# Kernel optimization log

Measured on AMD Instinct MI355X. Metric: run time of the kernel, lower is better.

## Reference

```python
import jax, jax.numpy as jnp
import numpy as np

C = 512
K = 3
DIL1 = 1  # dilation[0]
EPS = 1e-9


def _get_padding(kernel_size, dilation=1):
    return (kernel_size * dilation - dilation) // 2


def _upsample2_linear(x):
    # F.interpolate(x, scale_factor=2, mode='linear', align_corners=False)
    # x: [B, C, T] -> [B, C, 2T]
    T = x.shape[-1]
    coord = (jnp.arange(2 * T, dtype=x.dtype) + 0.5) * 0.5 - 0.5
    coord = jnp.maximum(coord, 0.0)  # PyTorch clamps source coord at 0
    i0 = jnp.floor(coord).astype(jnp.int32)
    i1 = jnp.minimum(i0 + 1, T - 1)
    w1 = coord - i0.astype(x.dtype)
    w0 = 1.0 - w1
    return x[..., i0] * w0 + x[..., i1] * w1


def _downsample2_avg(x):
    # AvgPool1d(kernel_size=2, stride=2)
    B, Ch, T = x.shape
    return x.reshape(B, Ch, T // 2, 2).mean(axis=-1)


def _snakebeta_act1d(x, alpha, beta):
    a = jnp.exp(alpha)[None, :, None]
    b = jnp.exp(beta)[None, :, None]
    up = _upsample2_linear(x)
    y = up + (1.0 - jnp.cos(2.0 * a * up)) / (2.0 * b + EPS)
    return _downsample2_avg(y)


def _wn_weight(v, g):
    # weight_norm: w = g * v / ||v||, norm over (in, k) dims per out channel
    norm = jnp.sqrt(jnp.sum(v * v, axis=(1, 2), keepdims=True))
    return g[:, None, None] * v / norm


def _conv1d(x, w, bias, dilation, pad):
    y = jax.lax.conv_general_dilated(
        x, w, window_strides=(1,), padding=[(pad, pad)],
        rhs_dilation=(dilation,), dimension_numbers=('NCH', 'OIH', 'NCH'))
    return y + bias[None, :, None]


def setup_inputs() -> dict:
    key = jax.random.key(0)
    ks = jax.random.split(key, 11)
    B, T = 8, 8192
    x = jax.random.normal(ks[0], (B, C, T), dtype=jnp.float32)
    v1 = jax.random.normal(ks[1], (C, C, K), dtype=jnp.float32) * 0.05
    g1 = jnp.ones((C,), dtype=jnp.float32)
    bias1 = jax.random.normal(ks[2], (C,), dtype=jnp.float32) * 0.01
    v2 = jax.random.normal(ks[3], (C, C, K), dtype=jnp.float32) * 0.05
    g2 = jnp.ones((C,), dtype=jnp.float32)
    bias2 = jax.random.normal(ks[4], (C,), dtype=jnp.float32) * 0.01
    # SnakeBeta logscale params (init 0 in torch; small random for testing)
    alpha1 = jax.random.normal(ks[5], (C,), dtype=jnp.float32) * 0.1
    beta1 = jax.random.normal(ks[6], (C,), dtype=jnp.float32) * 0.1
    alpha2 = jax.random.normal(ks[7], (C,), dtype=jnp.float32) * 0.1
    beta2 = jax.random.normal(ks[8], (C,), dtype=jnp.float32) * 0.1
    return {"x": x, "v1": v1, "g1": g1, "bias1": bias1,
            "v2": v2, "g2": g2, "bias2": bias2,
            "alpha1": alpha1, "beta1": beta1, "alpha2": alpha2, "beta2": beta2}


def reference(x, v1, g1, bias1, v2, g2, bias2, alpha1, beta1, alpha2, beta2):
    pad1 = _get_padding(K, DIL1)
    pad2 = _get_padding(K, 1)
    xt = _snakebeta_act1d(x, alpha1, beta1)
    xt = _conv1d(xt, _wn_weight(v1, g1), bias1, DIL1, pad1)
    xt = _snakebeta_act1d(xt, alpha2, beta2)
    xt = _conv1d(xt, _wn_weight(v2, g2), bias2, 1, pad2)
    return xt + x[:, :, :xt.shape[2]]
```

## Files before the change

### kernel.cpp

```cpp
#include <hip/hip_runtime.h>

typedef unsigned short ushort_t;
typedef __bf16 bf16x8 __attribute__((ext_vector_type(8)));
typedef float f32x4 __attribute__((ext_vector_type(4)));

#define B_  8
#define C_  512
#define T_  8192
#define TP_ 8194

static __device__ __forceinline__ float bf2f(ushort_t u) {
    return __uint_as_float(((unsigned)u) << 16);
}
static __device__ __forceinline__ ushort_t f2bf(float f) {
    unsigned u = __float_as_uint(f);
    unsigned r = (u + 0x7FFFu + ((u >> 16) & 1u)) >> 16;
    return (ushort_t)r;
}

static __device__ __forceinline__ void gl_lds16(const void* g, void* l) {
    __builtin_amdgcn_global_load_lds(
        (const __attribute__((address_space(1))) void*)g,
        (__attribute__((address_space(3))) void*)l, 16, 0, 0);
}

template <int BF> struct In;
template <> struct In<0> {
    static __device__ __forceinline__ float ld(const void* p, size_t i) {
        return ((const float*)p)[i];
    }
};
template <> struct In<1> {
    static __device__ __forceinline__ float ld(const void* p, size_t i) {
        return bf2f(((const ushort_t*)p)[i]);
    }
};

#define P_G1 0
#define P_B1 512
#define P_G2 1024
#define P_B2 1536
#define P_A1 2048
#define P_I1 2560
#define P_A2 3072
#define P_I2 3584

__global__ void param_kernel(const void* g1, const void* bias1, const void* g2, const void* bias2,
                             const void* alpha1, const void* beta1, const void* alpha2, const void* beta2,
                             float* __restrict__ pr, int* __restrict__ flag) {
    int i = threadIdx.x;
    unsigned guard = ((const unsigned*)g1)[0];
    int bf = (guard == 0x3F803F80u) ? 1 : 0;
    if (i == 0) *flag = bf;
    float g1v, b1v, g2v, b2v, a1v, be1v, a2v, be2v;
    if (bf) {
        g1v = In<1>::ld(g1, i);  b1v = In<1>::ld(bias1, i);
        g2v = In<1>::ld(g2, i);  b2v = In<1>::ld(bias2, i);
        a1v = In<1>::ld(alpha1, i); be1v = In<1>::ld(beta1, i);
        a2v = In<1>::ld(alpha2, i); be2v = In<1>::ld(beta2, i);
    } else {
        g1v = In<0>::ld(g1, i);  b1v = In<0>::ld(bias1, i);
        g2v = In<0>::ld(g2, i);  b2v = In<0>::ld(bias2, i);
        a1v = In<0>::ld(alpha1, i); be1v = In<0>::ld(beta1, i);
        a2v = In<0>::ld(alpha2, i); be2v = In<0>::ld(beta2, i);
    }
    pr[P_G1 + i] = g1v;
    pr[P_B1 + i] = b1v;
    pr[P_G2 + i] = g2v;
    pr[P_B2 + i] = b2v;
    pr[P_A1 + i] = __expf(a1v);
    pr[P_I1 + i] = 1.0f / (2.0f * __expf(be1v) + 1e-9f);
    pr[P_A2 + i] = __expf(a2v);
    pr[P_I2 + i] = 1.0f / (2.0f * __expf(be2v) + 1e-9f);
}

__global__ void wn_kernel(const void* __restrict__ v1, const void* __restrict__ v2,
                          const float* __restrict__ pr, const int* __restrict__ flag,
                          ushort_t* __restrict__ W1, ushort_t* __restrict__ W2) {
    int bf = *flag;
    const void* v = blockIdx.y ? v2 : v1;
    float g = pr[(blockIdx.y ? P_G2 : P_G1) + blockIdx.x];
    ushort_t* W = blockIdx.y ? W2 : W1;
    int co = blockIdx.x;
    int tid = threadIdx.x;
    size_t base = (size_t)co * 1536;
    float vals[6];
    float sum = 0.f;
    if (bf) {
        #pragma unroll
        for (int i = 0; i < 6; ++i) {
            float f = In<1>::ld(v, base + tid + i * 256);
            vals[i] = f;
            sum += f * f;
        }
    } else {
        #pragma unroll
        for (int i = 0; i < 6; ++i) {
            float f = In<0>::ld(v, base + tid + i * 256);
            vals[i] = f;
            sum += f * f;
        }
    }
    #pragma unroll
    for (int o = 32; o > 0; o >>= 1) sum += __shfl_down(sum, o, 64);
    __shared__ float red[4];
    if ((tid & 63) == 0) red[tid >> 6] = sum;
    __syncthreads();
    float tot = red[0] + red[1] + red[2] + red[3];
    float scale = g / sqrtf(tot);
    #pragma unroll
    for (int i = 0; i < 6; ++i) {
        int j = tid + i * 256;
        int cin = j / 3, k = j - cin * 3;
        W[(k * C_ + co) * C_ + cin] = f2bf(vals[i] * scale);
    }
}

__global__ void zero_pad_kernel(ushort_t* __restrict__ h) {
    int i = blockIdx.x * 256 + threadIdx.x;
    int b = i >> 10;
    int r = (i >> 9) & 1;
    int c = i & 511;
    h[((size_t)b * TP_ + (r ? (TP_ - 1) : 0)) * C_ + c] = 0;
}

__global__ void act1_kernel(const void* __restrict__ x,
                            const float* __restrict__ pr, const int* __restrict__ flag,
                            ushort_t* __restrict__ h) {
    __shared__ float s[64][65];
    int bf = *flag;
    int c0 = blockIdx.x * 64, t0 = blockIdx.y * 64, b = blockIdx.z;
    int tid = threadIdx.x;
    int cl = tid >> 2, seg = tid & 3;
    int c = c0 + cl;
    float a = pr[P_A1 + c];
    float inv2b = pr[P_I1 + c];
    size_t xbase = ((size_t)b * C_ + c) << 13;
    int tbase = t0 + seg * 16;
    float xv[18];
    if (bf) {
        const ushort_t* xp = (const ushort_t*)x + xbase;
        #pragma unroll
        for (int q = 0; q < 2; ++q) {
            uint4 v = *(const uint4*)(xp + tbase + q * 8);
            const ushort_t* pv = (const ushort_t*)&v;
            #pragma unroll
            for (int j = 0; j < 8; ++j) xv[1 + q * 8 + j] = bf2f(pv[j]);
        }
        xv[0]  = bf2f(xp[max(tbase - 1, 0)]);
        xv[17] = bf2f(xp[min(tbase + 16, T_ - 1)]);
    } else {
        const float* xp = (const float*)x + xbase;
        #pragma unroll
        for (int q = 0; q < 4; ++q) {
            float4 v = *(const float4*)(xp + tbase + q * 4);
            xv[1 + q * 4 + 0] = v.x;
            xv[1 + q * 4 + 1] = v.y;
            xv[1 + q * 4 + 2] = v.z;
            xv[1 + q * 4 + 3] = v.w;
        }
        xv[0]  = xp[max(tbase - 1, 0)];
        xv[17] = xp[min(tbase + 16, T_ - 1)];
    }
    #pragma unroll
    for (int j = 0; j < 16; ++j) {
        float xm = xv[j], xc = xv[j + 1], xp2 = xv[j + 2];
        float u0 = 0.25f * xm + 0.75f * xc;
        float u1 = 0.75f * xc + 0.25f * xp2;
        float s0 = u0 + (1.0f - __cosf(2.0f * a * u0)) * inv2b;
        float s1 = u1 + (1.0f - __cosf(2.0f * a * u1)) * inv2b;
        s[cl][seg * 16 + j] = 0.5f * (s0 + s1);
    }
    __syncthreads();
    int tl = tid >> 2;
    int t = t0 + tl;
    ushort_t* hrow = h + ((size_t)b * TP_ + (t + 1)) * C_ + c0 + seg * 16;
    #pragma unroll
    for (int q = 0; q < 4; ++q) {
        int cb = seg * 16 + q * 4;
        ushort4 w;
        w.x = f2bf(s[cb + 0][tl]);
        w.y = f2bf(s[cb + 1][tl]);
        w.z = f2bf(s[cb + 2][tl]);
        w.w = f2bf(s[cb + 3][tl]);
        *(ushort4*)(hrow + q * 4) = w;
    }
}

__global__ void act2_kernel(const ushort_t* __restrict__ z,
                            const float* __restrict__ pr,
                            ushort_t* __restrict__ h) {
    const int NV = B_ * T_ * (C_ / 8);
    int stride = gridDim.x * blockDim.x;
    for (int v = blockIdx.x * blockDim.x + threadIdx.x; v < NV; v += stride) {
        int c8 = v & 63;
        int t  = (v >> 6) & (T_ - 1);
        int b  = v >> 19;
        int c0 = c8 << 3;
        const ushort_t* zb = z + ((size_t)b << 22);
        uint4 vc = *(const uint4*)(zb + ((size_t)t << 9) + c0);
        uint4 vm = *(const uint4*)(zb + ((size_t)max(t - 1, 0) << 9) + c0);
        uint4 vp = *(const uint4*)(zb + ((size_t)min(t + 1, T_ - 1) << 9) + c0);
        float4 a0 = *(const float4*)(pr + P_A2 + c0);
        float4 a1 = *(const float4*)(pr + P_A2 + c0 + 4);
        float4 i0 = *(const float4*)(pr + P_I2 + c0);
        float4 i1 = *(const float4*)(pr + P_I2 + c0 + 4);
        float av[8] = {a0.x, a0.y, a0.z, a0.w, a1.x, a1.y, a1.z, a1.w};
        float iv[8] = {i0.x, i0.y, i0.z, i0.w, i1.x, i1.y, i1.z, i1.w};
        const ushort_t* pc = (const ushort_t*)&vc;
        const ushort_t* pm = (const ushort_t*)&vm;
        const ushort_t* pp = (const ushort_t*)&vp;
        ushort_t ov[8];
        #pragma unroll
        for (int j = 0; j < 8; ++j) {
            float zc = bf2f(pc[j]), zm = bf2f(pm[j]), zp = bf2f(pp[j]);
            float u0 = 0.25f * zm + 0.75f * zc;
            float u1 = 0.75f * zc + 0.25f * zp;
            float s0 = u0 + (1.0f - __cosf(2.0f * av[j] * u0)) * iv[j];
            float s1 = u1 + (1.0f - __cosf(2.0f * av[j] * u1)) * iv[j];
            ov[j] = f2bf(0.5f * (s0 + s1));
        }
        *(uint4*)(h + ((size_t)b * TP_ + t + 1) * C_ + c0) = *(const uint4*)ov;
    }
}

struct ConvAcc {
    f32x4 acc[4][4];
    int m0, t0, b, l15, qd, wm, wn;
};

static __device__ __forceinline__ void decode_blk(int& mB, int& tB, int& bB) {
    int id  = blockIdx.x + 4 * (blockIdx.y + 64 * blockIdx.z);
    int xcd = id & 7;
    int pos = id >> 3;
    bB  = pos >> 5;
    int w = pos & 31;
    mB  = w & 3;
    tB  = xcd * 8 + (w >> 2);
}

static __device__ __forceinline__ void conv_main(const ushort_t* __restrict__ Xt,
                                                 const ushort_t* __restrict__ W,
                                                 ConvAcc& S) {
    __shared__ __align__(16) ushort_t sA[3 * 128 * 32];
    __shared__ __align__(16) ushort_t sB[130 * 32];

    int tid = threadIdx.x;
    int lane = tid & 63, wid = tid >> 6;
    int wbase = tid & ~63;
    int mB, tB, bB;
    decode_blk(mB, tB, bB);
    S.m0 = mB * 128;
    S.t0 = tB * 128;
    S.b  = bB;
    S.wm = (wid >> 1) * 64;
    S.wn = (wid & 1) * 64;
    S.l15 = lane & 15;
    S.qd  = lane >> 4;
    #pragma unroll
    for (int mi = 0; mi < 4; ++mi)
        #pragma unroll
        for (int ni = 0; ni < 4; ++ni)
            S.acc[mi][ni] = (f32x4){0.f, 0.f, 0.f, 0.f};

    const ushort_t* xb = Xt + ((size_t)S.b * TP_ + S.t0) * C_;

    for (int ck = 0; ck < 16; ++ck) {
        int cin0 = ck * 32;
        #pragma unroll
        for (int i = 0; i < 6; ++i) {
            int idx = tid + i * 256;
            int tap = idx >> 9;
            int rem = idx & 511;
            int row = rem >> 2, part = rem & 3;
            const ushort_t* gp = W + (((size_t)((tap << 9) + S.m0 + row)) << 9) + cin0 + (part << 3);
            gl_lds16(gp, sA + (size_t)(i * 256 + wbase) * 8);
        }
        #pragma unroll
        for (int i = 0; i < 2; ++i) {
            int idx = tid + i * 256;
            int row = idx >> 2, part = idx & 3;
            const ushort_t* gp = xb + (size_t)row * C_ + cin0 + (part << 3);
            gl_lds16(gp, sB + (size_t)(i * 256 + wbase) * 8);
        }
        if (tid < 8) {
            int row = 128 + (tid >> 2), part = tid & 3;
            const uint4* gp = (const uint4*)(xb + (size_t)row * C_ + cin0 + (part << 3));
            *(uint4*)(sB + row * 32 + (part << 3)) = *gp;
        }
        __syncthreads();
        #pragma unroll
        for (int tap = 0; tap < 3; ++tap) {
            bf16x8 af[4], bfr[4];
            #pragma unroll
            for (int mi = 0; mi < 4; ++mi)
                af[mi] = *(const bf16x8*)(sA + tap * 4096 + (S.wm + mi * 16 + S.l15) * 32 + (S.qd << 3));
            #pragma unroll
            for (int ni = 0; ni < 4; ++ni)
                bfr[ni] = *(const bf16x8*)(sB + (S.wn + ni * 16 + S.l15 + tap) * 32 + (S.qd << 3));
            #pragma unroll
            for (int mi = 0; mi < 4; ++mi)
                #pragma unroll
                for (int ni = 0; ni < 4; ++ni)
                    S.acc[mi][ni] = __builtin_amdgcn_mfma_f32_16x16x32_bf16(af[mi], bfr[ni], S.acc[mi][ni], 0, 0, 0);
        }
        __syncthreads();
    }
}

__global__ __launch_bounds__(256) void conv1_kernel(const ushort_t* __restrict__ Xt,
                                                    const ushort_t* __restrict__ W,
                                                    const float* __restrict__ pr,
                                                    ushort_t* __restrict__ out) {
    ConvAcc S;
    conv_main(Xt, W, S);
    ushort_t* ob = out + ((size_t)S.b << 22);
    #pragma unroll
    for (int mi = 0; mi < 4; ++mi) {
        int cb = S.m0 + S.wm + mi * 16 + S.qd * 4;
        float b0 = pr[P_B1 + cb], b1 = pr[P_B1 + cb + 1];
        float b2 = pr[P_B1 + cb + 2], b3 = pr[P_B1 + cb + 3];
        #pragma unroll
        for (int ni = 0; ni < 4; ++ni) {
            int t = S.t0 + S.wn + ni * 16 + S.l15;
            ushort4 w;
            w.x = f2bf(S.acc[mi][ni][0] + b0);
            w.y = f2bf(S.acc[mi][ni][1] + b1);
            w.z = f2bf(S.acc[mi][ni][2] + b2);
            w.w = f2bf(S.acc[mi][ni][3] + b3);
            *(ushort4*)(ob + ((size_t)t << 9) + cb) = w;
        }
    }
}

__global__ __launch_bounds__(256) void conv2_kernel(const ushort_t* __restrict__ Xt,
                                                    const ushort_t* __restrict__ W,
                                                    const float* __restrict__ pr,
                                                    const int* __restrict__ flag,
                                                    const void* __restrict__ xres,
                                                    void* __restrict__ out) {
    int bf = *flag;
    ConvAcc S;
    conv_main(Xt, W, S);
    if (bf) {
        #pragma unroll
        for (int mi = 0; mi < 4; ++mi) {
            int cb = S.m0 + S.wm + mi * 16 + S.qd * 4;
            #pragma unroll
            for (int i = 0; i < 4; ++i) {
                float bi = pr[P_B2 + cb + i];
                size_t rowbase = ((size_t)S.b * C_ + cb + i) << 13;
                #pragma unroll
                for (int ni = 0; ni < 4; ++ni) {
                    int t = S.t0 + S.wn + ni * 16 + S.l15;
                    float val = S.acc[mi][ni][i] + bi + bf2f(((const ushort_t*)xres)[rowbase + t]);
                    ((ushort_t*)out)[rowbase + t] = f2bf(val);
                }
            }
        }
    } else {
        #pragma unroll
        for (int mi = 0; mi < 4; ++mi) {
            int cb = S.m0 + S.wm + mi * 16 + S.qd * 4;
            #pragma unroll
            for (int i = 0; i < 4; ++i) {
                float bi = pr[P_B2 + cb + i];
                size_t rowbase = ((size_t)S.b * C_ + cb + i) << 13;
                #pragma unroll
                for (int ni = 0; ni < 4; ++ni) {
                    int t = S.t0 + S.wn + ni * 16 + S.l15;
                    float val = S.acc[mi][ni][i] + bi + ((const float*)xres)[rowbase + t];
                    ((float*)out)[rowbase + t] = val;
                }
            }
        }
    }
}

extern "C" void kernel_launch(void* const* d_in, const int* in_sizes, int n_in,
                              void* d_out, int out_size, void* d_ws, size_t ws_size,
                              hipStream_t stream) {
    const void* x      = d_in[0];
    const void* v1     = d_in[1];
    const void* g1     = d_in[2];
    const void* bias1  = d_in[3];
    const void* v2     = d_in[4];
    const void* g2     = d_in[5];
    const void* bias2  = d_in[6];
    const void* alpha1 = d_in[7];
    const void* beta1  = d_in[8];
    const void* alpha2 = d_in[9];
    const void* beta2  = d_in[10];

    char* ws = (char*)d_ws;
    const size_t H_BYTES = (size_t)B_ * TP_ * C_ * 2;
    ushort_t* h_buf = (ushort_t*)ws;
    ushort_t* W1n   = (ushort_t*)(ws + H_BYTES);
    ushort_t* W2n   = W1n + 3 * C_ * C_;
    float*    pr    = (float*)(W2n + 3 * C_ * C_);
    int*      flag  = (int*)(pr + 8 * 512);
    ushort_t* z1 = (ushort_t*)d_out;

    param_kernel<<<1, 512, 0, stream>>>(g1, bias1, g2, bias2, alpha1, beta1, alpha2, beta2, pr, flag);
    wn_kernel<<<dim3(C_, 2), 256, 0, stream>>>(v1, v2, pr, flag, W1n, W2n);
    zero_pad_kernel<<<32, 256, 0, stream>>>(h_buf);
    act1_kernel<<<dim3(C_ / 64, T_ / 64, B_), 256, 0, stream>>>(x, pr, flag, h_buf);
    conv1_kernel<<<dim3(C_ / 128, T_ / 128, B_), 256, 0, stream>>>(h_buf, W1n, pr, z1);
    act2_kernel<<<2048, 256, 0, stream>>>(z1, pr, h_buf);
    conv2_kernel<<<dim3(C_ / 128, T_ / 128, B_), 256, 0, stream>>>(h_buf, W2n, pr, flag, x, d_out);
}
```

Before: 522.9 us.

## Stage conv1 epilogue through LDS and remap act kernels to XCD-contiguous tiles

The conv1 epilogue now writes its bf16 outputs into a shared-memory tile, then stores them as coalesced 16-byte rows instead of scattered 8-byte writes. act1 and act2 block indices are remapped so that consecutive blocks on the same XCD cover contiguous time ranges, which should improve L2 locality for neighbouring-time reads. act2 moves from a grid-stride loop to fixed 32-timestep chunks per block. The conv kernels share one LDS buffer, and conv1 pays an extra LDS round trip and a barrier in exchange.

```diff
diff --git a/kernel.cpp b/kernel.cpp
--- a/kernel.cpp
+++ b/kernel.cpp
@@ -129,7 +129,12 @@
                             ushort_t* __restrict__ h) {
     __shared__ float s[64][65];
     int bf = *flag;
-    int c0 = blockIdx.x * 64, t0 = blockIdx.y * 64, b = blockIdx.z;
+    int id = blockIdx.x + 8 * (blockIdx.y + 128 * blockIdx.z);
+    int xcd = id & 7;
+    int r   = id >> 3;
+    int b   = r >> 7;
+    int c0  = (r & 7) * 64;
+    int t0  = (xcd * 16 + ((r >> 3) & 15)) * 64;
     int tid = threadIdx.x;
     int cl = tid >> 2, seg = tid & 3;
     int c = c0 + cl;
@@ -190,14 +195,19 @@
 __global__ void act2_kernel(const ushort_t* __restrict__ z,
                             const float* __restrict__ pr,
                             ushort_t* __restrict__ h) {
-    const int NV = B_ * T_ * (C_ / 8);
-    int stride = gridDim.x * blockDim.x;
-    for (int v = blockIdx.x * blockDim.x + threadIdx.x; v < NV; v += stride) {
-        int c8 = v & 63;
-        int t  = (v >> 6) & (T_ - 1);
-        int b  = v >> 19;
-        int c0 = c8 << 3;
-        const ushort_t* zb = z + ((size_t)b << 22);
+    int id  = blockIdx.x;
+    int xcd = id & 7;
+    int r   = id >> 3;
+    int b   = r >> 5;
+    int tch = r & 31;
+    int t0  = xcd * 1024 + tch * 32;
+    int tid = threadIdx.x;
+    const ushort_t* zb = z + ((size_t)b << 22);
+    #pragma unroll
+    for (int k = 0; k < 8; ++k) {
+        int v = tid + k * 256;
+        int t = t0 + (v >> 6);
+        int c0 = (v & 63) << 3;
         uint4 vc = *(const uint4*)(zb + ((size_t)t << 9) + c0);
         uint4 vm = *(const uint4*)(zb + ((size_t)max(t - 1, 0) << 9) + c0);
         uint4 vp = *(const uint4*)(zb + ((size_t)min(t + 1, T_ - 1) << 9) + c0);
@@ -224,6 +234,8 @@
     }
 }
 
+#define SMEM_N 17408
+
 struct ConvAcc {
     f32x4 acc[4][4];
     int m0, t0, b, l15, qd, wm, wn;
@@ -241,9 +253,10 @@
 
 static __device__ __forceinline__ void conv_main(const ushort_t* __restrict__ Xt,
                                                  const ushort_t* __restrict__ W,
+                                                 ushort_t* smem,
                                                  ConvAcc& S) {
-    __shared__ __align__(16) ushort_t sA[3 * 128 * 32];
-    __shared__ __align__(16) ushort_t sB[130 * 32];
+    ushort_t* sA = smem;
+    ushort_t* sB = smem + 12288;
 
     int tid = threadIdx.x;
     int lane = tid & 63, wid = tid >> 6;
@@ -312,24 +325,36 @@
                                                     const ushort_t* __restrict__ W,
                                                     const float* __restrict__ pr,
                                                     ushort_t* __restrict__ out) {
+    __shared__ __align__(16) ushort_t smem[SMEM_N];
     ConvAcc S;
-    conv_main(Xt, W, S);
-    ushort_t* ob = out + ((size_t)S.b << 22);
+    conv_main(Xt, W, smem, S);
     #pragma unroll
     for (int mi = 0; mi < 4; ++mi) {
-        int cb = S.m0 + S.wm + mi * 16 + S.qd * 4;
+        int cl = S.wm + mi * 16 + S.qd * 4;
+        int cb = S.m0 + cl;
         float b0 = pr[P_B1 + cb], b1 = pr[P_B1 + cb + 1];
         float b2 = pr[P_B1 + cb + 2], b3 = pr[P_B1 + cb + 3];
         #pragma unroll
         for (int ni = 0; ni < 4; ++ni) {
-            int t = S.t0 + S.wn + ni * 16 + S.l15;
+            int tl = S.wn + ni * 16 + S.l15;
             ushort4 w;
             w.x = f2bf(S.acc[mi][ni][0] + b0);
             w.y = f2bf(S.acc[mi][ni][1] + b1);
             w.z = f2bf(S.acc[mi][ni][2] + b2);
             w.w = f2bf(S.acc[mi][ni][3] + b3);
-            *(ushort4*)(ob + ((size_t)t << 9) + cb) = w;
-        }
+            *(ushort4*)(smem + tl * 136 + cl) = w;
+        }
+    }
+    __syncthreads();
+    ushort_t* ob = out + ((size_t)S.b << 22);
+    int tid = threadIdx.x;
+    #pragma unroll
+    for (int k = 0; k < 8; ++k) {
+        int id = tid + k * 256;
+        int r  = id >> 4;
+        int c8 = id & 15;
+        uint4 v = *(const uint4*)(smem + r * 136 + (c8 << 3));
+        *(uint4*)(ob + ((size_t)(S.t0 + r) << 9) + S.m0 + (c8 << 3)) = v;
     }
 }
 
@@ -339,9 +364,10 @@
                                                     const int* __restrict__ flag,
                                                     const void* __restrict__ xres,
                                                     void* __restrict__ out) {
+    __shared__ __align__(16) ushort_t smem[SMEM_N];
     int bf = *flag;
     ConvAcc S;
-    conv_main(Xt, W, S);
+    conv_main(Xt, W, smem, S);
     if (bf) {
         #pragma unroll
         for (int mi = 0; mi < 4; ++mi) {
@@ -404,7 +430,7 @@
     param_kernel<<<1, 512, 0, stream>>>(g1, bias1, g2, bias2, alpha1, beta1, alpha2, beta2, pr, flag);
     wn_kernel<<<dim3(C_, 2), 256, 0, stream>>>(v1, v2, pr, flag, W1n, W2n);
     zero_pad_kernel<<<32, 256, 0, stream>>>(h_buf);
-    act1_kernel<<<dim3(C_ / 64, T_ / 64, B_), 256, 0, stream>>>(x, pr, flag, h_buf);
+    act1_kernel<<<dim3(8, 128, 8), 256, 0, stream>>>(x, pr, flag, h_buf);
     conv1_kernel<<<dim3(C_ / 128, T_ / 128, B_), 256, 0, stream>>>(h_buf, W1n, pr, z1);
     act2_kernel<<<2048, 256, 0, stream>>>(z1, pr, h_buf);
     conv2_kernel<<<dim3(C_ / 128, T_ / 128, B_), 256, 0, stream>>>(h_buf, W2n, pr, flag, x, d_out);
```

New measurement: 514.7 us. Within noise of the previous version (-1.6%).
